# Kernel tuning notes

Measured on AMD Instinct MI355X. Metric: run time of the kernel, lower is better.

Reference implementation:

```python
import jax, jax.numpy as jnp
import numpy as np

TEMPERATURE = 0.5
EPS = 1e-8  # torch CosineSimilarity default eps


def setup_inputs() -> dict:
    key = jax.random.key(0)
    k1, k2 = jax.random.split(key)
    N, D = 4096, 256
    return {
        "batch_embeddings": jax.random.normal(k1, (N, D), dtype=jnp.float32),
        "batch_augmented_embeddings": jax.random.normal(k2, (N, D), dtype=jnp.float32),
    }


def reference(batch_embeddings, batch_augmented_embeddings):
    N = batch_embeddings.shape[0]
    emb = jnp.concatenate([batch_embeddings, batch_augmented_embeddings], axis=0)  # (2N, D)
    # cosine similarity = normalized dot products (normalize + GEMM rewrite of the
    # broadcasted nn.CosineSimilarity)
    norms = jnp.sqrt(jnp.sum(emb * emb, axis=-1, keepdims=True))
    emb_n = emb / jnp.maximum(norms, EPS)
    sim = jnp.einsum("id,jd->ij", emb_n, emb_n) / TEMPERATURE  # (2N, 2N)
    # negative mask: (~eye(N)).repeat(2,2) -> False where (i mod N) == (j mod N)
    idx = jnp.arange(2 * N)
    neg_mask = (idx[:, None] % N) != (idx[None, :] % N)
    exp_sim = jnp.exp(sim) * neg_mask.astype(sim.dtype)
    sum_exp = jnp.sum(exp_sim, axis=-1)  # (2N,)
    pos = jnp.arange(N)
    positive_sim = sim[pos, N + pos]  # (N,)
    negative_sim_sum = sum_exp[:N]  # (N,)
    loss = -jnp.mean(jnp.log(jnp.exp(positive_sim) / negative_sim_sum))
    return loss
```

## Files before the change

kernel.cpp:

```cpp
#include <hip/hip_runtime.h>
#include <hip/hip_bf16.h>

#define NROWS 4096
#define DDIM  256
#define EPS   1e-8f
#define SCALE 1.69864944f
#define LN2   0.69314718056f

#define NJ 32
#define JS 256
#define BT 64
#define CH (JS / BT)
#define BUFSH (4 * 8 * 64 * 8)

typedef __attribute__((ext_vector_type(8))) short short8;
typedef __attribute__((ext_vector_type(4))) float f32x4;

#if __has_builtin(__builtin_amdgcn_exp2f)
#define EXP2F(x) __builtin_amdgcn_exp2f(x)
#else
#define EXP2F(x) exp2f(x)
#endif

__device__ __forceinline__ unsigned short f2bf(float x) {
    union { __hip_bfloat16 h; unsigned short u; } c;
    c.h = __float2bfloat16(x);
    return c.u;
}
__device__ __forceinline__ float bf2f(unsigned short u) {
    union { unsigned int i; float f; } c;
    c.i = ((unsigned int)u) << 16;
    return c.f;
}

__global__ void normalize_kernel(const float* __restrict__ a,
                                 const float* __restrict__ b,
                                 unsigned short* __restrict__ en,
                                 float* __restrict__ S,
                                 float* __restrict__ cell,
                                 unsigned int* __restrict__ counter, int N) {
    const int wave = threadIdx.x >> 6, lane = threadIdx.x & 63;
    const int row = blockIdx.x * 4 + wave;
    const float* src = (row < N) ? (a + (size_t)row * DDIM)
                                 : (b + (size_t)(row - N) * DDIM);
    const float4 v = reinterpret_cast<const float4*>(src)[lane];
    float ss = v.x * v.x + v.y * v.y + v.z * v.z + v.w * v.w;
    #pragma unroll
    for (int off = 32; off > 0; off >>= 1) ss += __shfl_xor(ss, off);
    const float inv = SCALE / fmaxf(sqrtf(ss), EPS * SCALE);
    ushort4 o;
    o.x = f2bf(v.x * inv);
    o.y = f2bf(v.y * inv);
    o.z = f2bf(v.z * inv);
    o.w = f2bf(v.w * inv);
    *reinterpret_cast<ushort4*>(en + (size_t)row * DDIM + lane * 4) = o;
    if (lane == 0 && row < N) S[row] = 0.0f;
    if (blockIdx.x == 0 && threadIdx.x == 0) { *cell = 0.0f; *counter = 0u; }
}

__global__ __launch_bounds__(256, 2) void simsum_kernel(
        const short* __restrict__ en,
        float* __restrict__ S) {
    __shared__ short bt[2 * BUFSH];
    const int tid = threadIdx.x;
    const int wave = tid >> 6, lane = tid & 63;
    const int lrow = lane & 15, quad = lane >> 4;
    const int i0 = blockIdx.x * 256 + wave * 64;
    const int jb = blockIdx.y * JS;

    auto stage = [&](int jc, int buf) {
        const short* g = en + (size_t)(jc + wave * 16 + lrow) * DDIM + quad * 8;
        short* l = bt + buf * BUFSH + wave * 4096;
        #pragma unroll
        for (int ks = 0; ks < 8; ++ks) {
            __builtin_amdgcn_global_load_lds(
                (const __attribute__((address_space(1))) void*)(g + ks * 32),
                (__attribute__((address_space(3))) void*)(l + ks * 512),
                16, 0, 0);
        }
    };

    stage(jb, 0);

    short8 afrag[4][8];
    #pragma unroll
    for (int t = 0; t < 4; ++t)
        #pragma unroll
        for (int ks = 0; ks < 8; ++ks)
            afrag[t][ks] = *reinterpret_cast<const short8*>(
                en + (size_t)(i0 + t * 16 + lrow) * DDIM + ks * 32 + quad * 8);

    float rowsum[4][4];
    #pragma unroll
    for (int t = 0; t < 4; ++t)
        #pragma unroll
        for (int r = 0; r < 4; ++r) rowsum[t][r] = 0.0f;

    for (int c = 0; c < CH; ++c) {
        __syncthreads();
        if (c + 1 < CH) stage(jb + (c + 1) * BT, (c + 1) & 1);
        const short* lb = bt + (c & 1) * BUFSH;
        #pragma unroll
        for (int cg = 0; cg < 4; ++cg) {
            f32x4 acc[4];
            #pragma unroll
            for (int t = 0; t < 4; ++t) acc[t] = f32x4{0.f, 0.f, 0.f, 0.f};
            #pragma unroll
            for (int ks = 0; ks < 8; ++ks) {
                const short8 bfrag = *reinterpret_cast<const short8*>(
                    lb + cg * 4096 + ks * 512 + lane * 8);
                #pragma unroll
                for (int t = 0; t < 4; ++t)
                    acc[t] = __builtin_amdgcn_mfma_f32_16x16x32_bf16(
                        afrag[t][ks], bfrag, acc[t], 0, 0, 0);
            }
            #pragma unroll
            for (int t = 0; t < 4; ++t)
                #pragma unroll
                for (int r = 0; r < 4; ++r)
                    rowsum[t][r] += EXP2F(acc[t][r]);
        }
    }

    #pragma unroll
    for (int t = 0; t < 4; ++t) {
        #pragma unroll
        for (int r = 0; r < 4; ++r) {
            float v = rowsum[t][r];
            v += __shfl_xor(v, 1);
            v += __shfl_xor(v, 2);
            v += __shfl_xor(v, 4);
            v += __shfl_xor(v, 8);
            rowsum[t][r] = v;
        }
        if (lrow < 4) {
            const float v = (lrow == 0) ? rowsum[t][0]
                          : (lrow == 1) ? rowsum[t][1]
                          : (lrow == 2) ? rowsum[t][2]
                          :               rowsum[t][3];
            atomicAdd(&S[i0 + t * 16 + quad * 4 + lrow], v);
        }
    }
}

__global__ void loss_kernel(const unsigned short* __restrict__ en,
                            const float* __restrict__ S,
                            float* __restrict__ cell,
                            unsigned int* __restrict__ counter,
                            float* __restrict__ out, int N) {
    const int tid = threadIdx.x;
    const int wave = tid >> 6, lane = tid & 63;
    const int gw = blockIdx.x * 4 + wave;
    float wacc = 0.0f;
    for (int rr = 0; rr < 16; ++rr) {
        const int row = gw * 16 + rr;
        const ushort4 ua = *reinterpret_cast<const ushort4*>(
            en + (size_t)row * DDIM + lane * 4);
        const ushort4 ub = *reinterpret_cast<const ushort4*>(
            en + (size_t)(N + row) * DDIM + lane * 4);
        const float a0 = bf2f(ua.x), a1 = bf2f(ua.y),
                    a2 = bf2f(ua.z), a3 = bf2f(ua.w);
        const float b0 = bf2f(ub.x), b1 = bf2f(ub.y),
                    b2 = bf2f(ub.z), b3 = bf2f(ub.w);
        float sd = a0 * a0 + a1 * a1 + a2 * a2 + a3 * a3;
        float pd = a0 * b0 + a1 * b1 + a2 * b2 + a3 * b3;
        #pragma unroll
        for (int off = 32; off > 0; off >>= 1) {
            sd += __shfl_xor(sd, off);
            pd += __shfl_xor(pd, off);
        }
        if (lane == 0) {
            const float Sc = S[row] - EXP2F(sd) - EXP2F(pd);
            wacc += pd * LN2 - LN2 * __log2f(Sc);
        }
    }
    __shared__ float bs[4];
    if (lane == 0) bs[wave] = wacc;
    __syncthreads();
    if (tid == 0) {
        atomicAdd(cell, bs[0] + bs[1] + bs[2] + bs[3]);
        __threadfence();
        const unsigned int old = atomicAdd(counter, 1u);
        if (old == gridDim.x - 1) {
            const float tot = atomicAdd(cell, 0.0f);
            out[0] = -tot / (float)N;
        }
    }
}

extern "C" void kernel_launch(void* const* d_in, const int* in_sizes, int n_in,
                              void* d_out, int out_size, void* d_ws, size_t ws_size,
                              hipStream_t stream) {
    const float* a = (const float*)d_in[0];
    const float* b = (const float*)d_in[1];
    float* out = (float*)d_out;
    const int N = NROWS;

    char* ws = (char*)d_ws;
    unsigned short* en = (unsigned short*)ws;
    float* S = (float*)(ws + (size_t)2 * N * DDIM * sizeof(unsigned short));
    float* cell = S + N;
    unsigned int* counter = (unsigned int*)(cell + 1);

    normalize_kernel<<<(2 * N) / 4, 256, 0, stream>>>(a, b, en, S, cell,
                                                      counter, N);
    simsum_kernel<<<dim3(N / 256, NJ), 256, 0, stream>>>((const short*)en, S);
    loss_kernel<<<64, 256, 0, stream>>>(en, S, cell, counter, out, N);
}
```

Baseline: 106.2 us.

## Switch similarity GEMM to 32x32x16 MFMA tiles with matching LDS layout

Replaces the 16x16x32 bf16 MFMA tiling (4 row tiles x 4 column groups per wave) with 32x32x16 MFMA (2 row tiles x 2 column groups). The LDS staging layout, A-fragment loads and the row-sum reduction/atomic scatter are reorganized to match the 32x32 output layout. The aim is fewer instructions and less LDS fragment traffic per FLOP thanks to the larger MFMA shape. In exchange, A-fragment and accumulator register pressure changes (afrag is now 2x16 short8), which may affect occupancy under launch_bounds(256,2).

```diff
diff --git a/kernel.cpp b/kernel.cpp
--- a/kernel.cpp
+++ b/kernel.cpp
@@ -11,10 +11,10 @@
 #define JS 256
 #define BT 64
 #define CH (JS / BT)
-#define BUFSH (4 * 8 * 64 * 8)
+#define BUFSH (2 * 16 * 512)
 
 typedef __attribute__((ext_vector_type(8))) short short8;
-typedef __attribute__((ext_vector_type(4))) float f32x4;
+typedef __attribute__((ext_vector_type(16))) float f32x16;
 
 #if __has_builtin(__builtin_amdgcn_exp2f)
 #define EXP2F(x) __builtin_amdgcn_exp2f(x)
@@ -64,81 +64,82 @@
     __shared__ short bt[2 * BUFSH];
     const int tid = threadIdx.x;
     const int wave = tid >> 6, lane = tid & 63;
-    const int lrow = lane & 15, quad = lane >> 4;
+    const int l31 = lane & 31, half = lane >> 5;
     const int i0 = blockIdx.x * 256 + wave * 64;
     const int jb = blockIdx.y * JS;
 
     auto stage = [&](int jc, int buf) {
-        const short* g = en + (size_t)(jc + wave * 16 + lrow) * DDIM + quad * 8;
-        short* l = bt + buf * BUFSH + wave * 4096;
-        #pragma unroll
-        for (int ks = 0; ks < 8; ++ks) {
+        const int cg = wave & 1;
+        const int kb = wave >> 1;
+        const short* g = en + (size_t)(jc + cg * 32 + l31) * DDIM
+                            + kb * 128 + half * 8;
+        short* l = bt + buf * BUFSH + cg * 8192 + kb * 4096;
+        #pragma unroll
+        for (int i = 0; i < 8; ++i) {
             __builtin_amdgcn_global_load_lds(
-                (const __attribute__((address_space(1))) void*)(g + ks * 32),
-                (__attribute__((address_space(3))) void*)(l + ks * 512),
+                (const __attribute__((address_space(1))) void*)(g + i * 16),
+                (__attribute__((address_space(3))) void*)(l + i * 512),
                 16, 0, 0);
         }
     };
 
     stage(jb, 0);
 
-    short8 afrag[4][8];
-    #pragma unroll
-    for (int t = 0; t < 4; ++t)
-        #pragma unroll
-        for (int ks = 0; ks < 8; ++ks)
+    short8 afrag[2][16];
+    #pragma unroll
+    for (int t = 0; t < 2; ++t)
+        #pragma unroll
+        for (int ks = 0; ks < 16; ++ks)
             afrag[t][ks] = *reinterpret_cast<const short8*>(
-                en + (size_t)(i0 + t * 16 + lrow) * DDIM + ks * 32 + quad * 8);
-
-    float rowsum[4][4];
-    #pragma unroll
-    for (int t = 0; t < 4; ++t)
-        #pragma unroll
-        for (int r = 0; r < 4; ++r) rowsum[t][r] = 0.0f;
+                en + (size_t)(i0 + t * 32 + l31) * DDIM + ks * 16 + half * 8);
+
+    float rowsum[2][16];
+    #pragma unroll
+    for (int t = 0; t < 2; ++t)
+        #pragma unroll
+        for (int r = 0; r < 16; ++r) rowsum[t][r] = 0.0f;
 
     for (int c = 0; c < CH; ++c) {
         __syncthreads();
         if (c + 1 < CH) stage(jb + (c + 1) * BT, (c + 1) & 1);
         const short* lb = bt + (c & 1) * BUFSH;
         #pragma unroll
-        for (int cg = 0; cg < 4; ++cg) {
-            f32x4 acc[4];
+        for (int cg = 0; cg < 2; ++cg) {
+            f32x16 acc[2];
             #pragma unroll
-            for (int t = 0; t < 4; ++t) acc[t] = f32x4{0.f, 0.f, 0.f, 0.f};
+            for (int t = 0; t < 2; ++t)
+                #pragma unroll
+                for (int r = 0; r < 16; ++r) acc[t][r] = 0.0f;
             #pragma unroll
-            for (int ks = 0; ks < 8; ++ks) {
+            for (int ks = 0; ks < 16; ++ks) {
                 const short8 bfrag = *reinterpret_cast<const short8*>(
-                    lb + cg * 4096 + ks * 512 + lane * 8);
+                    lb + cg * 8192 + ks * 512 + lane * 8);
                 #pragma unroll
-                for (int t = 0; t < 4; ++t)
-                    acc[t] = __builtin_amdgcn_mfma_f32_16x16x32_bf16(
+                for (int t = 0; t < 2; ++t)
+                    acc[t] = __builtin_amdgcn_mfma_f32_32x32x16_bf16(
                         afrag[t][ks], bfrag, acc[t], 0, 0, 0);
             }
             #pragma unroll
-            for (int t = 0; t < 4; ++t)
+            for (int t = 0; t < 2; ++t)
                 #pragma unroll
-                for (int r = 0; r < 4; ++r)
+                for (int r = 0; r < 16; ++r)
                     rowsum[t][r] += EXP2F(acc[t][r]);
         }
     }
 
     #pragma unroll
-    for (int t = 0; t < 4; ++t) {
-        #pragma unroll
-        for (int r = 0; r < 4; ++r) {
+    for (int t = 0; t < 2; ++t) {
+        #pragma unroll
+        for (int r = 0; r < 16; ++r) {
             float v = rowsum[t][r];
             v += __shfl_xor(v, 1);
             v += __shfl_xor(v, 2);
             v += __shfl_xor(v, 4);
             v += __shfl_xor(v, 8);
-            rowsum[t][r] = v;
-        }
-        if (lrow < 4) {
-            const float v = (lrow == 0) ? rowsum[t][0]
-                          : (lrow == 1) ? rowsum[t][1]
-                          : (lrow == 2) ? rowsum[t][2]
-                          :               rowsum[t][3];
-            atomicAdd(&S[i0 + t * 16 + quad * 4 + lrow], v);
+            v += __shfl_xor(v, 16);
+            if (l31 == r)
+                atomicAdd(&S[i0 + t * 32 + (r & 3) + 8 * (r >> 2) + 4 * half],
+                          v);
         }
     }
 }
```

Result: slower. 126.1 us (+18.7%).

## Shrink simsum tile to 128 rows per block for higher occupancy

Applied to the files above, without the earlier changes.

Each wave now handles 32 query rows instead of 64, each block covers 128 rows, and the column chunk staged in LDS drops to 32 rows. The grid doubles, launch bounds rise to 4 blocks per CU, and staging is spread across all waves. The goal is more waves in flight and less register pressure to hide latency. In exchange, each staged B tile is reused by fewer A rows, so global/LDS traffic per MFMA doubles and there are more barriers per unit of work.

```diff
diff --git a/kernel.cpp b/kernel.cpp
--- a/kernel.cpp
+++ b/kernel.cpp
@@ -9,9 +9,9 @@
 
 #define NJ 32
 #define JS 256
-#define BT 64
+#define BT 32
 #define CH (JS / BT)
-#define BUFSH (4 * 8 * 64 * 8)
+#define BUFSH (2 * 8 * 512)
 
 typedef __attribute__((ext_vector_type(8))) short short8;
 typedef __attribute__((ext_vector_type(4))) float f32x4;
@@ -58,41 +58,43 @@
     if (blockIdx.x == 0 && threadIdx.x == 0) { *cell = 0.0f; *counter = 0u; }
 }
 
-__global__ __launch_bounds__(256, 2) void simsum_kernel(
+__global__ __launch_bounds__(256, 4) void simsum_kernel(
         const short* __restrict__ en,
         float* __restrict__ S) {
     __shared__ short bt[2 * BUFSH];
     const int tid = threadIdx.x;
     const int wave = tid >> 6, lane = tid & 63;
     const int lrow = lane & 15, quad = lane >> 4;
-    const int i0 = blockIdx.x * 256 + wave * 64;
+    const int i0 = blockIdx.x * 128 + wave * 32;
     const int jb = blockIdx.y * JS;
 
     auto stage = [&](int jc, int buf) {
-        const short* g = en + (size_t)(jc + wave * 16 + lrow) * DDIM + quad * 8;
-        short* l = bt + buf * BUFSH + wave * 4096;
-        #pragma unroll
-        for (int ks = 0; ks < 8; ++ks) {
+        #pragma unroll
+        for (int i = 0; i < 4; ++i) {
+            const int c2 = wave * 4 + i;
+            const int cg = c2 >> 3, ks = c2 & 7;
+            const short* g = en + (size_t)(jc + cg * 16 + lrow) * DDIM
+                                + ks * 32 + quad * 8;
+            short* l = bt + buf * BUFSH + c2 * 512;
             __builtin_amdgcn_global_load_lds(
-                (const __attribute__((address_space(1))) void*)(g + ks * 32),
-                (__attribute__((address_space(3))) void*)(l + ks * 512),
-                16, 0, 0);
+                (const __attribute__((address_space(1))) void*)g,
+                (__attribute__((address_space(3))) void*)l, 16, 0, 0);
         }
     };
 
     stage(jb, 0);
 
-    short8 afrag[4][8];
-    #pragma unroll
-    for (int t = 0; t < 4; ++t)
+    short8 afrag[2][8];
+    #pragma unroll
+    for (int t = 0; t < 2; ++t)
         #pragma unroll
         for (int ks = 0; ks < 8; ++ks)
             afrag[t][ks] = *reinterpret_cast<const short8*>(
                 en + (size_t)(i0 + t * 16 + lrow) * DDIM + ks * 32 + quad * 8);
 
-    float rowsum[4][4];
-    #pragma unroll
-    for (int t = 0; t < 4; ++t)
+    float rowsum[2][4];
+    #pragma unroll
+    for (int t = 0; t < 2; ++t)
         #pragma unroll
         for (int r = 0; r < 4; ++r) rowsum[t][r] = 0.0f;
 
@@ -101,29 +103,28 @@
         if (c + 1 < CH) stage(jb + (c + 1) * BT, (c + 1) & 1);
         const short* lb = bt + (c & 1) * BUFSH;
         #pragma unroll
-        for (int cg = 0; cg < 4; ++cg) {
-            f32x4 acc[4];
-            #pragma unroll
-            for (int t = 0; t < 4; ++t) acc[t] = f32x4{0.f, 0.f, 0.f, 0.f};
+        for (int cg = 0; cg < 2; ++cg) {
+            f32x4 acc0 = {0.f, 0.f, 0.f, 0.f};
+            f32x4 acc1 = {0.f, 0.f, 0.f, 0.f};
             #pragma unroll
             for (int ks = 0; ks < 8; ++ks) {
                 const short8 bfrag = *reinterpret_cast<const short8*>(
                     lb + cg * 4096 + ks * 512 + lane * 8);
-                #pragma unroll
-                for (int t = 0; t < 4; ++t)
-                    acc[t] = __builtin_amdgcn_mfma_f32_16x16x32_bf16(
-                        afrag[t][ks], bfrag, acc[t], 0, 0, 0);
+                acc0 = __builtin_amdgcn_mfma_f32_16x16x32_bf16(
+                    afrag[0][ks], bfrag, acc0, 0, 0, 0);
+                acc1 = __builtin_amdgcn_mfma_f32_16x16x32_bf16(
+                    afrag[1][ks], bfrag, acc1, 0, 0, 0);
             }
             #pragma unroll
-            for (int t = 0; t < 4; ++t)
-                #pragma unroll
-                for (int r = 0; r < 4; ++r)
-                    rowsum[t][r] += EXP2F(acc[t][r]);
-        }
-    }
-
-    #pragma unroll
-    for (int t = 0; t < 4; ++t) {
+            for (int r = 0; r < 4; ++r) {
+                rowsum[0][r] += EXP2F(acc0[r]);
+                rowsum[1][r] += EXP2F(acc1[r]);
+            }
+        }
+    }
+
+    #pragma unroll
+    for (int t = 0; t < 2; ++t) {
         #pragma unroll
         for (int r = 0; r < 4; ++r) {
             float v = rowsum[t][r];
@@ -204,6 +205,6 @@
 
     normalize_kernel<<<(2 * N) / 4, 256, 0, stream>>>(a, b, en, S, cell,
                                                       counter, N);
-    simsum_kernel<<<dim3(N / 256, NJ), 256, 0, stream>>>((const short*)en, S);
+    simsum_kernel<<<dim3(N / 128, NJ), 256, 0, stream>>>((const short*)en, S);
     loss_kernel<<<64, 256, 0, stream>>>(en, S, cell, counter, out, N);
 }
```

After: 127.2 us. 19.7% more time.

## Pre-swizzle normalized embeddings into MFMA fragment layout, load B directly from global

Applied to the files above, without the earlier changes.

The normalize kernel now also writes a second copy of the bf16 embeddings laid out in MFMA fragment order. The simsum kernel drops its LDS double-buffered staging and __syncthreads, and streams B fragments straight from global (L2/L1) into registers with a two-half software prefetch. Each load is contiguous per lane. This removes LDS traffic and barriers, but each wave now fetches the full B tile independently, which raises global/cache traffic and register pressure. It also needs an extra workspace buffer and an extra write in normalize.

```diff
diff --git a/kernel.cpp b/kernel.cpp
--- a/kernel.cpp
+++ b/kernel.cpp
@@ -9,9 +9,6 @@
 
 #define NJ 32
 #define JS 256
-#define BT 64
-#define CH (JS / BT)
-#define BUFSH (4 * 8 * 64 * 8)
 
 typedef __attribute__((ext_vector_type(8))) short short8;
 typedef __attribute__((ext_vector_type(4))) float f32x4;
@@ -36,6 +33,7 @@
 __global__ void normalize_kernel(const float* __restrict__ a,
                                  const float* __restrict__ b,
                                  unsigned short* __restrict__ en,
+                                 unsigned short* __restrict__ gfrag,
                                  float* __restrict__ S,
                                  float* __restrict__ cell,
                                  unsigned int* __restrict__ counter, int N) {
@@ -54,41 +52,31 @@
     o.z = f2bf(v.z * inv);
     o.w = f2bf(v.w * inv);
     *reinterpret_cast<ushort4*>(en + (size_t)row * DDIM + lane * 4) = o;
+    const int ks = lane >> 3, quad = (lane >> 1) & 3, e = (lane & 1) * 4;
+    const size_t fo = (size_t)(row >> 4) * 4096 + ks * 512
+                      + (quad * 16 + (row & 15)) * 8 + e;
+    *reinterpret_cast<ushort4*>(gfrag + fo) = o;
     if (lane == 0 && row < N) S[row] = 0.0f;
     if (blockIdx.x == 0 && threadIdx.x == 0) { *cell = 0.0f; *counter = 0u; }
 }
 
 __global__ __launch_bounds__(256, 2) void simsum_kernel(
-        const short* __restrict__ en,
+        const short* __restrict__ gfrag,
         float* __restrict__ S) {
-    __shared__ short bt[2 * BUFSH];
     const int tid = threadIdx.x;
     const int wave = tid >> 6, lane = tid & 63;
     const int lrow = lane & 15, quad = lane >> 4;
     const int i0 = blockIdx.x * 256 + wave * 64;
     const int jb = blockIdx.y * JS;
 
-    auto stage = [&](int jc, int buf) {
-        const short* g = en + (size_t)(jc + wave * 16 + lrow) * DDIM + quad * 8;
-        short* l = bt + buf * BUFSH + wave * 4096;
-        #pragma unroll
-        for (int ks = 0; ks < 8; ++ks) {
-            __builtin_amdgcn_global_load_lds(
-                (const __attribute__((address_space(1))) void*)(g + ks * 32),
-                (__attribute__((address_space(3))) void*)(l + ks * 512),
-                16, 0, 0);
-        }
-    };
-
-    stage(jb, 0);
-
     short8 afrag[4][8];
     #pragma unroll
     for (int t = 0; t < 4; ++t)
         #pragma unroll
         for (int ks = 0; ks < 8; ++ks)
             afrag[t][ks] = *reinterpret_cast<const short8*>(
-                en + (size_t)(i0 + t * 16 + lrow) * DDIM + ks * 32 + quad * 8);
+                gfrag + (size_t)(blockIdx.x * 16 + wave * 4 + t) * 4096
+                      + ks * 512 + lane * 8);
 
     float rowsum[4][4];
     #pragma unroll
@@ -96,30 +84,46 @@
         #pragma unroll
         for (int r = 0; r < 4; ++r) rowsum[t][r] = 0.0f;
 
-    for (int c = 0; c < CH; ++c) {
-        __syncthreads();
-        if (c + 1 < CH) stage(jb + (c + 1) * BT, (c + 1) & 1);
-        const short* lb = bt + (c & 1) * BUFSH;
-        #pragma unroll
-        for (int cg = 0; cg < 4; ++cg) {
-            f32x4 acc[4];
-            #pragma unroll
-            for (int t = 0; t < 4; ++t) acc[t] = f32x4{0.f, 0.f, 0.f, 0.f};
-            #pragma unroll
-            for (int ks = 0; ks < 8; ++ks) {
-                const short8 bfrag = *reinterpret_cast<const short8*>(
-                    lb + cg * 4096 + ks * 512 + lane * 8);
-                #pragma unroll
-                for (int t = 0; t < 4; ++t)
-                    acc[t] = __builtin_amdgcn_mfma_f32_16x16x32_bf16(
-                        afrag[t][ks], bfrag, acc[t], 0, 0, 0);
-            }
+    const short* bptr = gfrag + (size_t)(jb >> 4) * 4096 + lane * 8;
+    short8 bf0[4], bf1[4];
+
+    #pragma unroll
+    for (int k4 = 0; k4 < 4; ++k4)
+        bf0[k4] = *reinterpret_cast<const short8*>(bptr + k4 * 512);
+
+    for (int g = 0; g < 16; ++g) {
+        const short* gb = bptr + g * 4096;
+        #pragma unroll
+        for (int k4 = 0; k4 < 4; ++k4)
+            bf1[k4] = *reinterpret_cast<const short8*>(gb + 2048 + k4 * 512);
+
+        f32x4 acc[4];
+        #pragma unroll
+        for (int t = 0; t < 4; ++t) acc[t] = f32x4{0.f, 0.f, 0.f, 0.f};
+        #pragma unroll
+        for (int k4 = 0; k4 < 4; ++k4)
             #pragma unroll
             for (int t = 0; t < 4; ++t)
-                #pragma unroll
-                for (int r = 0; r < 4; ++r)
-                    rowsum[t][r] += EXP2F(acc[t][r]);
-        }
+                acc[t] = __builtin_amdgcn_mfma_f32_16x16x32_bf16(
+                    afrag[t][k4], bf0[k4], acc[t], 0, 0, 0);
+
+        if (g + 1 < 16) {
+            #pragma unroll
+            for (int k4 = 0; k4 < 4; ++k4)
+                bf0[k4] = *reinterpret_cast<const short8*>(gb + 4096 + k4 * 512);
+        }
+        #pragma unroll
+        for (int k4 = 0; k4 < 4; ++k4)
+            #pragma unroll
+            for (int t = 0; t < 4; ++t)
+                acc[t] = __builtin_amdgcn_mfma_f32_16x16x32_bf16(
+                    afrag[t][4 + k4], bf1[k4], acc[t], 0, 0, 0);
+
+        #pragma unroll
+        for (int t = 0; t < 4; ++t)
+            #pragma unroll
+            for (int r = 0; r < 4; ++r)
+                rowsum[t][r] += EXP2F(acc[t][r]);
     }
 
     #pragma unroll
@@ -198,12 +202,13 @@
 
     char* ws = (char*)d_ws;
     unsigned short* en = (unsigned short*)ws;
-    float* S = (float*)(ws + (size_t)2 * N * DDIM * sizeof(unsigned short));
+    unsigned short* gfrag = en + (size_t)2 * N * DDIM;
+    float* S = (float*)(gfrag + (size_t)2 * N * DDIM);
     float* cell = S + N;
     unsigned int* counter = (unsigned int*)(cell + 1);
 
-    normalize_kernel<<<(2 * N) / 4, 256, 0, stream>>>(a, b, en, S, cell,
-                                                      counter, N);
-    simsum_kernel<<<dim3(N / 256, NJ), 256, 0, stream>>>((const short*)en, S);
+    normalize_kernel<<<(2 * N) / 4, 256, 0, stream>>>(a, b, en, gfrag, S,
+                                                      cell, counter, N);
+    simsum_kernel<<<dim3(N / 256, NJ), 256, 0, stream>>>((const short*)gfrag, S);
     loss_kernel<<<64, 256, 0, stream>>>(en, S, cell, counter, out, N);
 }
```

New measurement: 166.8 us. 1.57x slower.
